# Optimization experiments

Measured on AMD Instinct MI355X. Metric: run time of the kernel, lower is better.

Reference implementation:

```python
import jax, jax.numpy as jnp
import numpy as np

B, S, E, H, D, W = 2, 4096, 768, 12, 64, 256  # batch, seq, hidden, heads, head_dim, one-sided window


def setup_inputs() -> dict:
    key = jax.random.key(0)
    ks = jax.random.split(key, 4)
    s = 0.02
    return {
        "hidden_states": jax.random.normal(ks[0], (B, S, E), jnp.float32),
        "Wq": jax.random.normal(ks[1], (E, E), jnp.float32) * s,
        "bq": jnp.zeros((E,), jnp.float32),
        "Wk": jax.random.normal(ks[2], (E, E), jnp.float32) * s,
        "bk": jnp.zeros((E,), jnp.float32),
        "Wv": jax.random.normal(ks[3], (E, E), jnp.float32) * s,
        "bv": jnp.zeros((E,), jnp.float32),
    }


def _band_attention(q, k, v):
    # q,k,v: [B,H,S,D]. Sliding-window attention: query i attends keys j with |j-i| <= W,
    # clipped to [0, S) -- same math as sliding_chunks_matmul_qk + mask_invalid_locations
    # + softmax + sliding_chunks_matmul_pv (dropout p=0, eval mode).
    C = S // W  # number of query chunks of size W

    def ext(x):
        # gather, for each chunk c, the keys of chunks c-1, c, c+1 (zero padded at edges)
        xp = jnp.pad(x, ((0, 0), (0, 0), (W, W), (0, 0)))
        xc = xp.reshape(B, H, C + 2, W, D)
        return jnp.concatenate([xc[:, :, 0:C], xc[:, :, 1:C + 1], xc[:, :, 2:C + 2]], axis=3)  # [B,H,C,3W,D]

    qc = q.reshape(B, H, C, W, D)
    ke = ext(k)
    ve = ext(v)
    scores = jnp.einsum('bhcpd,bhctd->bhcpt', qc, ke)  # [B,H,C,W,3W]

    p = jnp.arange(W)[:, None]            # query offset within chunk
    t = jnp.arange(3 * W)[None, :]        # key offset within extended window
    rel = t - W - p                       # j - i  (relative position)
    j = jnp.arange(C)[:, None, None] * W + (t - W)[None]  # global key index [C,W,3W]
    mask = (jnp.abs(rel)[None] <= W) & (j >= 0) & (j < S)  # band + sequence-boundary mask

    scores = jnp.where(mask[None, None], scores, -1e30)
    probs = jax.nn.softmax(scores, axis=-1)
    out = jnp.einsum('bhcpt,bhctd->bhcpd', probs, ve)
    return out.reshape(B, H, S, D)


def reference(hidden_states, Wq, bq, Wk, bk, Wv, bv):
    scale = 1.0 / float(np.sqrt(D))
    q = (hidden_states @ Wq + bq) * scale  # q scaled by 1/sqrt(head_dim) as in original
    k = hidden_states @ Wk + bk
    v = hidden_states @ Wv + bv
    split = lambda x: x.reshape(B, S, H, D).transpose(0, 2, 1, 3)  # [B,H,S,D]
    out = _band_attention(split(q), split(k), split(v))
    return out.transpose(0, 2, 1, 3).reshape(B, S, E)  # [B,S,E] context_layer
```

## Files before the change

kernel.cpp:

```cpp
#include <hip/hip_runtime.h>

#define BB 2
#define SS 4096
#define EE 768
#define HH 12
#define DD 64
#define WW 256

typedef __attribute__((ext_vector_type(8))) short short8;
typedef __attribute__((ext_vector_type(4))) short short4v;
typedef __attribute__((ext_vector_type(4))) float floatx4;

#define MFMA16(a, b, c) __builtin_amdgcn_mfma_f32_16x16x32_bf16(a, b, c, 0, 0, 0)

__device__ __forceinline__ float bf2f(short x) {
    union { unsigned u; float f; } v;
    v.u = ((unsigned)(unsigned short)x) << 16;
    return v.f;
}

__device__ __forceinline__ short f2bf(float x) {
    union { float f; unsigned u; } v;
    v.f = x;
    unsigned r = v.u + 0x7fffu + ((v.u >> 16) & 1u);
    return (short)(r >> 16);
}

__device__ __forceinline__ int imin(int a, int b) { return a < b ? a : b; }
__device__ __forceinline__ int imax(int a, int b) { return a > b ? a : b; }

__device__ __forceinline__ void gload_lds16(const short* g, short* l) {
    __builtin_amdgcn_global_load_lds(
        (const __attribute__((address_space(1))) unsigned*)g,
        (__attribute__((address_space(3))) unsigned*)l, 16, 0, 0);
}

__global__ __launch_bounds__(256) void prep(
    const float* __restrict__ hidden, const float* __restrict__ W0,
    const float* __restrict__ W1, const float* __restrict__ W2,
    short* __restrict__ Xb, short* __restrict__ Wt) {
    __shared__ short t[32][33];
    int bid = blockIdx.x;
    if (bid < 3072) {
        int i = bid * 256 + threadIdx.x;
        const floatx4* src = (const floatx4*)(hidden + (size_t)i * 8);
        floatx4 f0 = src[0], f1 = src[1];
        short8 s8;
#pragma unroll
        for (int j = 0; j < 4; j++) { s8[j] = f2bf(f0[j]); s8[j + 4] = f2bf(f1[j]); }
        *(short8*)(Xb + (size_t)i * 8) = s8;
    } else {
        int tmp = bid - 3072;
        int z = tmp / 576, r = tmp % 576;
        int bx = r % 24, by = r / 24;
        const float* in = (z == 0) ? W0 : (z == 1) ? W1 : W2;
        short* op = Wt + (size_t)z * EE * EE;
        int tx = threadIdx.x & 31, ty = threadIdx.x >> 5;
        int x = bx * 32 + tx, y0 = by * 32;
        for (int j = 0; j < 32; j += 8) t[ty + j][tx] = f2bf(in[(size_t)(y0 + ty + j) * EE + x]);
        __syncthreads();
        int x2 = y0 + tx, y2 = bx * 32;
        for (int j = 0; j < 32; j += 8) op[(size_t)(y2 + ty + j) * EE + x2] = t[tx][ty + j];
    }
}

__global__ __launch_bounds__(256) void qkv_gemm(
    const short* __restrict__ Xb, const short* __restrict__ Wt,
    const float* __restrict__ Bq, const float* __restrict__ Bk, const float* __restrict__ Bv,
    short* __restrict__ Qo, short* __restrict__ Ko, short* __restrict__ Vto) {
    int z = blockIdx.z;
    const short* Wz = Wt + (size_t)z * EE * EE;
    const float* bias = (z == 0) ? Bq : (z == 1) ? Bk : Bv;

    __shared__ __align__(16) short As[128 * 32];
    __shared__ __align__(16) short Bs[128 * 32];
    int tid = threadIdx.x;
    int m0 = blockIdx.x * 128, n0 = blockIdx.y * 128;
    int wave = tid >> 6, lane = tid & 63, lquad = lane >> 4, lrow = lane & 15;
    int wm = (wave & 1) * 64, wn = (wave >> 1) * 64;

    floatx4 acc[4][4] = {};

    int c0 = tid, c1 = 256 + tid;
    int r0s = c0 >> 2, c0s = (c0 & 3) * 8;
    int r1s = c1 >> 2, c1s = (c1 & 3) * 8;

    for (int k0 = 0; k0 < EE; k0 += 32) {
        gload_lds16(&Xb[(size_t)(m0 + r0s) * EE + k0 + c0s], &As[c0 * 8]);
        gload_lds16(&Wz[(size_t)(n0 + r0s) * EE + k0 + c0s], &Bs[c0 * 8]);
        gload_lds16(&Xb[(size_t)(m0 + r1s) * EE + k0 + c1s], &As[c1 * 8]);
        gload_lds16(&Wz[(size_t)(n0 + r1s) * EE + k0 + c1s], &Bs[c1 * 8]);
        __syncthreads();
        short8 af[4], bfv[4];
#pragma unroll
        for (int mt = 0; mt < 4; mt++)
            af[mt] = *(short8*)&As[(wm + mt * 16 + lrow) * 32 + lquad * 8];
#pragma unroll
        for (int nt = 0; nt < 4; nt++)
            bfv[nt] = *(short8*)&Bs[(wn + nt * 16 + lrow) * 32 + lquad * 8];
#pragma unroll
        for (int mt = 0; mt < 4; mt++)
#pragma unroll
            for (int nt = 0; nt < 4; nt++)
                acc[mt][nt] = MFMA16(af[mt], bfv[nt], acc[mt][nt]);
        __syncthreads();
    }

    if (z == 2) {
        for (int nt = 0; nt < 4; nt++) {
            int gn = n0 + wn + nt * 16 + lrow;
            float bv = bias[gn];
            int h = gn >> 6, d = gn & 63;
            for (int mt = 0; mt < 4; mt++) {
                int gm0 = m0 + wm + mt * 16 + lquad * 4;
                int b = gm0 >> 12, s = gm0 & (SS - 1);
                short4v pk;
                for (int r = 0; r < 4; r++) pk[r] = f2bf(acc[mt][nt][r] + bv);
                *(short4v*)&Vto[(((size_t)(b * HH + h)) * DD + d) * SS + s] = pk;
            }
        }
    } else {
        short* out = (z == 0) ? Qo : Ko;
        float scale = (z == 0) ? 0.125f : 1.0f;
        for (int nt = 0; nt < 4; nt++) {
            int gn = n0 + wn + nt * 16 + lrow;
            float bv = bias[gn];
            int h = gn >> 6, d = gn & 63;
            for (int mt = 0; mt < 4; mt++) {
                int gmb = m0 + wm + mt * 16 + lquad * 4;
                for (int r = 0; r < 4; r++) {
                    int gm = gmb + r;
                    int b = gm >> 12, s = gm & (SS - 1);
                    float v = (acc[mt][nt][r] + bv) * scale;
                    out[(((size_t)(b * HH + h)) * SS + s) * DD + d] = f2bf(v);
                }
            }
        }
    }
}

__global__ __launch_bounds__(256) void band_attn(
    const short* __restrict__ Q, const short* __restrict__ K,
    const short* __restrict__ Vt, float* __restrict__ out) {
    int hb = blockIdx.x;
    int h = hb % HH, b = hb / HH;
    int chunk = blockIdx.y;
    int tid = threadIdx.x;
    int wave = tid >> 6, lane = tid & 63, lquad = lane >> 4, lrow = lane & 15;
    int qbase = chunk * 128 + wave * 32;

    const short* Qh = Q + ((size_t)(b * HH + h)) * SS * DD;
    const short* Kh = K + ((size_t)(b * HH + h)) * SS * DD;
    const short* Vh = Vt + ((size_t)(b * HH + h)) * DD * SS;

    __shared__ __align__(16) short Ks[2][64 * 72];
    __shared__ __align__(16) short Vs[2][64 * 72];
    __shared__ __align__(16) short Ps[4][16 * 72];
    short* Pw = &Ps[wave][0];

    short8 qf[2][2];
#pragma unroll
    for (int m = 0; m < 2; m++)
#pragma unroll
        for (int hh = 0; hh < 2; hh++)
            qf[m][hh] = *(const short8*)&Qh[(size_t)(qbase + m * 16 + lrow) * DD + hh * 32 + lquad * 8];

    floatx4 o[2][4] = {};
    float ls[2] = {0.0f, 0.0f};

    int kwin = chunk * 128 - WW;
    int srow = tid >> 3;
    int scol = (tid & 7) * 8;
    int tlo = wave >> 1;

    short8 kreg[2], vreg[2];
    auto loadTile = [&](int t) {
        int ks0 = kwin + t * 64;
#pragma unroll
        for (int i = 0; i < 2; i++) {
            int r = srow + i * 32;
            int gk = imin(imax(ks0 + r, 0), SS - 1);
            kreg[i] = *(const short8*)&Kh[(size_t)gk * DD + scol];
            int gv = imin(imax(ks0 + scol, 0), SS - 8);
            vreg[i] = *(const short8*)&Vh[(size_t)r * SS + gv];
        }
    };
    auto storeTile = [&](int buf) {
#pragma unroll
        for (int i = 0; i < 2; i++) {
            int r = srow + i * 32;
            *(short8*)&Ks[buf][r * 72 + scol] = kreg[i];
            *(short8*)&Vs[buf][r * 72 + scol] = vreg[i];
        }
    };

    loadTile(0);
    storeTile(0);
    __syncthreads();

    for (int t = 0; t < 10; t++) {
        int buf = t & 1;
        if (t < 9) loadTile(t + 1);

        if ((unsigned)(t - tlo) < 9u) {
            int ks0 = kwin + t * 64;
            short8 kf[4][2], vf[4][2];
#pragma unroll
            for (int kt = 0; kt < 4; kt++)
#pragma unroll
                for (int hh = 0; hh < 2; hh++)
                    kf[kt][hh] = *(short8*)&Ks[buf][(kt * 16 + lrow) * 72 + hh * 32 + lquad * 8];
#pragma unroll
            for (int nt = 0; nt < 4; nt++)
#pragma unroll
                for (int hh = 0; hh < 2; hh++)
                    vf[nt][hh] = *(short8*)&Vs[buf][(nt * 16 + lrow) * 72 + hh * 32 + lquad * 8];

            int d0 = ks0 - qbase;
            bool interior = (d0 >= -225) && (d0 <= 193) && (ks0 >= 0) && (ks0 <= SS - 64);

#pragma unroll
            for (int m = 0; m < 2; m++) {
                int q = qbase + m * 16 + lrow;
                floatx4 s[4];
#pragma unroll
                for (int kt = 0; kt < 4; kt++) {
                    floatx4 zz = {};
                    s[kt] = MFMA16(kf[kt][0], qf[m][0], zz);
                    s[kt] = MFMA16(kf[kt][1], qf[m][1], s[kt]);
                }
                float lacc = 0.0f;
                if (interior) {
#pragma unroll
                    for (int kt = 0; kt < 4; kt++) {
                        short4v pk;
#pragma unroll
                        for (int r = 0; r < 4; r++) {
                            float p = __expf(s[kt][r]);
                            pk[r] = f2bf(p);
                            lacc += bf2f(pk[r]);
                        }
                        *(short4v*)&Pw[lrow * 72 + kt * 16 + lquad * 4] = pk;
                    }
                } else {
#pragma unroll
                    for (int kt = 0; kt < 4; kt++) {
                        short4v pk;
#pragma unroll
                        for (int r = 0; r < 4; r++) {
                            int key = ks0 + kt * 16 + lquad * 4 + r;
                            bool valid = ((unsigned)(key - q + WW) <= 2u * WW) && ((unsigned)key < SS);
                            float p = valid ? __expf(s[kt][r]) : 0.0f;
                            pk[r] = f2bf(p);
                            lacc += bf2f(pk[r]);
                        }
                        *(short4v*)&Pw[lrow * 72 + kt * 16 + lquad * 4] = pk;
                    }
                }
                ls[m] += lacc;
                asm volatile("" ::: "memory");
                short8 ap0 = *(short8*)&Pw[lrow * 72 + lquad * 8];
                short8 ap1 = *(short8*)&Pw[lrow * 72 + 32 + lquad * 8];
#pragma unroll
                for (int nt = 0; nt < 4; nt++) {
                    o[m][nt] = MFMA16(ap0, vf[nt][0], o[m][nt]);
                    o[m][nt] = MFMA16(ap1, vf[nt][1], o[m][nt]);
                }
            }
        }

        if (t < 9) storeTile(buf ^ 1);
        __syncthreads();
    }

#pragma unroll
    for (int m = 0; m < 2; m++) {
        ls[m] += __shfl_xor(ls[m], 16, 64);
        ls[m] += __shfl_xor(ls[m], 32, 64);
        ls[m] = 1.0f / ls[m];
    }

#pragma unroll
    for (int m = 0; m < 2; m++) {
#pragma unroll
        for (int r = 0; r < 4; r++) {
            float linv = __shfl(ls[m], lquad * 4 + r, 64);
            int s = qbase + m * 16 + lquad * 4 + r;
#pragma unroll
            for (int nt = 0; nt < 4; nt++)
                out[((size_t)b * SS + s) * EE + h * DD + nt * 16 + lrow] = o[m][nt][r] * linv;
        }
    }
}

extern "C" void kernel_launch(void* const* d_in, const int* in_sizes, int n_in,
                              void* d_out, int out_size, void* d_ws, size_t ws_size,
                              hipStream_t stream) {
    const float* hidden = (const float*)d_in[0];
    const float* Wq = (const float*)d_in[1];
    const float* bq = (const float*)d_in[2];
    const float* Wk = (const float*)d_in[3];
    const float* bk = (const float*)d_in[4];
    const float* Wv = (const float*)d_in[5];
    const float* bv = (const float*)d_in[6];
    float* out = (float*)d_out;

    short* ws = (short*)d_ws;
    const size_t WSZ = (size_t)EE * EE;
    const size_t QSZ = (size_t)BB * HH * SS * DD;
    short* Wt = ws;
    short* Qb = Wt + 3 * WSZ;
    short* Kb = Qb + QSZ;
    short* Vtb = Kb + QSZ;
    short* Xb = (short*)d_out;

    prep<<<dim3(3072 + 3 * 576, 1, 1), 256, 0, stream>>>(hidden, Wq, Wk, Wv, Xb, Wt);

    qkv_gemm<<<dim3(64, 6, 3), 256, 0, stream>>>(Xb, Wt, bq, bk, bv, Qb, Kb, Vtb);

    band_attn<<<dim3(HH * BB, SS / 128, 1), 256, 0, stream>>>(Qb, Kb, Vtb, out);
}
```

Before: 181.3 us.

## Triple-buffer LDS tiles in QKV GEMM to overlap loads with MFMA

The QKV projection GEMM's K loop changes from single-buffered global-to-LDS loads with two barriers per iteration to a three-deep LDS ring. The next tile is prefetched before computing the current one, and vmcnt waits plus a single barrier replace the syncthreads. This is meant to hide global load latency behind MFMA work and remove one barrier per step. In exchange LDS use triples, which could reduce occupancy, and correctness depends on the hand-counted vmcnt values and the three-buffer reuse distance.

```diff
diff --git a/kernel.cpp b/kernel.cpp
--- a/kernel.cpp
+++ b/kernel.cpp
@@ -72,8 +72,8 @@
     const short* Wz = Wt + (size_t)z * EE * EE;
     const float* bias = (z == 0) ? Bq : (z == 1) ? Bk : Bv;
 
-    __shared__ __align__(16) short As[128 * 32];
-    __shared__ __align__(16) short Bs[128 * 32];
+    __shared__ __align__(16) short As[3][128 * 32];
+    __shared__ __align__(16) short Bs[3][128 * 32];
     int tid = threadIdx.x;
     int m0 = blockIdx.x * 128, n0 = blockIdx.y * 128;
     int wave = tid >> 6, lane = tid & 63, lquad = lane >> 4, lrow = lane & 15;
@@ -85,25 +85,37 @@
     int r0s = c0 >> 2, c0s = (c0 & 3) * 8;
     int r1s = c1 >> 2, c1s = (c1 & 3) * 8;
 
-    for (int k0 = 0; k0 < EE; k0 += 32) {
-        gload_lds16(&Xb[(size_t)(m0 + r0s) * EE + k0 + c0s], &As[c0 * 8]);
-        gload_lds16(&Wz[(size_t)(n0 + r0s) * EE + k0 + c0s], &Bs[c0 * 8]);
-        gload_lds16(&Xb[(size_t)(m0 + r1s) * EE + k0 + c1s], &As[c1 * 8]);
-        gload_lds16(&Wz[(size_t)(n0 + r1s) * EE + k0 + c1s], &Bs[c1 * 8]);
-        __syncthreads();
+    auto stage = [&](int k0, int buf) {
+        gload_lds16(&Xb[(size_t)(m0 + r0s) * EE + k0 + c0s], &As[buf][c0 * 8]);
+        gload_lds16(&Wz[(size_t)(n0 + r0s) * EE + k0 + c0s], &Bs[buf][c0 * 8]);
+        gload_lds16(&Xb[(size_t)(m0 + r1s) * EE + k0 + c1s], &As[buf][c1 * 8]);
+        gload_lds16(&Wz[(size_t)(n0 + r1s) * EE + k0 + c1s], &Bs[buf][c1 * 8]);
+    };
+
+    stage(0, 0);
+    int buf = 0, nbuf = 1;
+    for (int i = 0; i < 24; i++) {
+        if (i < 23) {
+            stage((i + 1) * 32, nbuf);
+            asm volatile("s_waitcnt vmcnt(4)" ::: "memory");
+        } else {
+            asm volatile("s_waitcnt vmcnt(0)" ::: "memory");
+        }
+        asm volatile("s_barrier" ::: "memory");
         short8 af[4], bfv[4];
 #pragma unroll
         for (int mt = 0; mt < 4; mt++)
-            af[mt] = *(short8*)&As[(wm + mt * 16 + lrow) * 32 + lquad * 8];
+            af[mt] = *(short8*)&As[buf][(wm + mt * 16 + lrow) * 32 + lquad * 8];
 #pragma unroll
         for (int nt = 0; nt < 4; nt++)
-            bfv[nt] = *(short8*)&Bs[(wn + nt * 16 + lrow) * 32 + lquad * 8];
+            bfv[nt] = *(short8*)&Bs[buf][(wn + nt * 16 + lrow) * 32 + lquad * 8];
 #pragma unroll
         for (int mt = 0; mt < 4; mt++)
 #pragma unroll
             for (int nt = 0; nt < 4; nt++)
                 acc[mt][nt] = MFMA16(af[mt], bfv[nt], acc[mt][nt]);
-        __syncthreads();
+        buf = nbuf;
+        nbuf = (nbuf == 2) ? 0 : nbuf + 1;
     }
 
     if (z == 2) {
```

Result: no change. 182.2 us (+0.5%).
